# Optimization experiments

Measured on AMD Instinct MI355X. Metric: run time of the kernel, lower is better.

## Reference

```python
import jax, jax.numpy as jnp
import numpy as np
import math

NEG = -1e9
NUM_SQUEEZE = 2


def seq_mask(lengths, max_len, dtype):
    return (jnp.arange(max_len)[None, :] < lengths[:, None]).astype(dtype)


def maximum_path(logp, attn_mask, x_lengths, y_lengths):
    """Monotonic alignment search (Viterbi DP). logp, attn_mask: [B, Tx, Ty]."""
    B, Tx, Ty = logp.shape
    logp = jnp.where(attn_mask > 0, logp, NEG)
    cols = jnp.moveaxis(logp, 2, 0)  # [Ty, B, Tx]

    v0 = jnp.where(jnp.arange(Tx)[None, :] == 0, 0.0, NEG).astype(logp.dtype)
    v0 = jnp.broadcast_to(v0, (B, Tx))

    def fwd(v, col):
        v_shift = jnp.concatenate([jnp.full((B, 1), NEG, logp.dtype), v[:, :-1]], axis=1)
        v_new = col + jnp.maximum(v, v_shift)
        return v_new, v_new

    _, values = jax.lax.scan(fwd, v0, cols)  # [Ty, B, Tx] DP table

    def bwd(index, j):
        active = j < y_lengths  # [B]
        row = jax.nn.one_hot(index, Tx, dtype=logp.dtype) * active[:, None].astype(logp.dtype)
        vprev = values[jnp.maximum(j - 1, 0)]  # [B, Tx]
        v_here = jnp.take_along_axis(vprev, index[:, None], axis=1)[:, 0]
        v_left = jnp.take_along_axis(vprev, jnp.maximum(index - 1, 0)[:, None], axis=1)[:, 0]
        dec = (index != 0) & ((index == j) | (v_here < v_left)) & active & (j > 0)
        return jnp.where(dec, index - 1, index), row

    js = jnp.arange(Ty - 1, -1, -1)
    _, rows = jax.lax.scan(bwd, x_lengths - 1, js)  # reversed j order
    path = jnp.moveaxis(jnp.flip(rows, 0), 0, 2)  # [B, Tx, Ty]
    return path * attn_mask


def setup_inputs() -> dict:
    key = jax.random.key(0)
    ks = jax.random.split(key, 6)
    B, C, Ten, Tde = 32, 80, 512, 2048
    return {
        "o_mean": jax.random.normal(ks[0], (B, C, Ten), jnp.float32),
        "o_log_scale": jax.random.normal(ks[1], (B, C, Ten), jnp.float32) * 0.1,
        "o_dur_log": jax.random.normal(ks[2], (B, 1, Ten), jnp.float32),
        "z": jax.random.normal(ks[3], (B, C, Tde), jnp.float32),
        "x_lengths": jax.random.randint(ks[4], (B,), Ten // 2, Ten + 1, jnp.int32),
        "y_lengths": jax.random.randint(ks[5], (B,), Tde // 2, Tde + 1, jnp.int32),
    }


def reference(o_mean, o_log_scale, o_dur_log, z, x_lengths, y_lengths):
    B, C, Ten = o_mean.shape
    Tde = z.shape[2]
    dt = o_mean.dtype

    # preprocess: floor y_lengths to multiple of num_squeeze
    y_lengths = (y_lengths // NUM_SQUEEZE) * NUM_SQUEEZE

    x_mask = seq_mask(x_lengths, Ten, dt)[:, None, :]   # [B,1,Tx]
    y_mask = seq_mask(y_lengths, Tde, dt)[:, None, :]   # [B,1,Ty]
    attn_mask = x_mask[:, 0, :, None] * y_mask[:, 0, None, :]  # [B,Tx,Ty]

    z = z * y_mask  # decoder output is masked

    # log-likelihood terms (torch.no_grad in original)
    o_scale = jnp.exp(-2.0 * o_log_scale)                       # [B,C,Tx]
    logp1 = jnp.sum(-0.5 * math.log(2 * math.pi) - o_log_scale, axis=1)[:, :, None]
    logp2 = jnp.einsum('bct,bcs->bts', o_scale, -0.5 * z * z)   # [B,Tx,Ty]
    logp3 = jnp.einsum('bct,bcs->bts', o_mean * o_scale, z)
    logp4 = jnp.sum(-0.5 * o_mean * o_mean * o_scale, axis=1)[:, :, None]
    logp = logp1 + logp2 + logp3 + logp4

    attn = maximum_path(logp, attn_mask, x_lengths, y_lengths)  # [B,Tx,Ty] hard path

    # compute_outputs
    y_mean = jnp.einsum('bts,bct->bcs', attn, o_mean)           # [B,C,Ty]
    y_log_scale = jnp.einsum('bts,bct->bcs', attn, o_log_scale)
    o_attn_dur = jnp.log1p(jnp.sum(attn, axis=-1))[:, None, :] * x_mask  # [B,1,Tx]

    return (
        jnp.transpose(z, (0, 2, 1)),            # z: [B,Ty,C]
        jnp.transpose(y_mean, (0, 2, 1)),       # y_mean: [B,Ty,C]
        jnp.transpose(y_log_scale, (0, 2, 1)),  # y_log_scale: [B,Ty,C]
        jnp.transpose(attn, (0, 2, 1)),         # alignments: [B,Ty,Tx]
        jnp.transpose(o_dur_log, (0, 2, 1)),    # durations_log: [B,Tx,1]
        jnp.transpose(o_attn_dur, (0, 2, 1)),   # total_durations_log: [B,Tx,1]
    )
```

## Files before the change

kernel.cpp:

```cpp
#include <hip/hip_runtime.h>
#include <math.h>

#define BB  32
#define CC  80
#define TXX 512
#define TYY 2048
#define NEGV -1e9f

typedef float v2f __attribute__((ext_vector_type(2)));

__global__ __launch_bounds__(256) void k_prep(
    const float* __restrict__ om, const float* __restrict__ ols,
    float* __restrict__ SA, float* __restrict__ SB,
    float* __restrict__ L1, float* __restrict__ L4,
    float* __restrict__ OMTf, float* __restrict__ OLSTf)
{
    int b = blockIdx.y;
    int t0 = blockIdx.x * 64;
    int tid = threadIdx.x;
    int cl = tid >> 6;
    int tl = tid & 63;
    __shared__ float sm[64][81], sl[64][81], ssa[64][81];
    #pragma unroll
    for (int cp = 0; cp < 20; ++cp) {
        int c = cp * 4 + cl;
        size_t gidx = ((size_t)b * CC + c) * TXX + t0 + tl;
        float m = om[gidx], ls = ols[gidx];
        float sa = expf(-2.0f * ls);
        SA[gidx] = sa;
        SB[gidx] = m * sa;
        sm[tl][c] = m; sl[tl][c] = ls; ssa[tl][c] = sa;
    }
    __syncthreads();
    if (tid < 64) {
        float l1 = 0.f, l4 = 0.f;
        #pragma unroll 4
        for (int c = 0; c < CC; ++c) {
            float m = sm[tid][c], ls = sl[tid][c], sa = ssa[tid][c];
            l1 += (-0.9189385332046727f - ls);
            l4 += ((-0.5f * m) * m) * sa;
        }
        int g = b * TXX + t0 + tid;
        L1[g] = l1; L4[g] = l4;
    }
    size_t obase = (size_t)b * TXX * CC + (size_t)t0 * CC;
    for (int e = tid; e < 64 * CC; e += 256) {
        int t = e / CC, c = e - t * CC;
        OMTf[obase + e]  = sm[t][c];
        OLSTf[obase + e] = sl[t][c];
    }
}

__global__ __launch_bounds__(256) void k_logp(
    const float* __restrict__ SA, const float* __restrict__ SB,
    const float* __restrict__ L1, const float* __restrict__ L4,
    const float* __restrict__ z,
    const int* __restrict__ xlp, const int* __restrict__ ylp,
    float* __restrict__ logp)
{
    int b = blockIdx.z;
    int ylen = (ylp[b] >> 1) << 1;
    int s0 = blockIdx.y * 128;
    if (s0 >= ylen) return;
    int t0 = blockIdx.x * 64;
    int xlen = xlp[b];
    int tid = threadIdx.x;

    __shared__ float sA[16][64], sB[16][64], sZ[16][128], sW[16][128];

    v2f acc2[4][4], acc3[4][4];
    #pragma unroll
    for (int i = 0; i < 4; ++i)
        #pragma unroll
        for (int p = 0; p < 4; ++p) { acc2[i][p] = (v2f){0.f, 0.f}; acc3[i][p] = (v2f){0.f, 0.f}; }

    int tt = (tid & 15) << 2;
    int ss = (tid >> 4) << 3;
    int r  = tid >> 4;
    int c4 = (tid & 15) << 2;
    int s8 = (tid & 15) << 3;

    for (int c0 = 0; c0 < CC; c0 += 16) {
        const float* pa = SA + ((size_t)b * CC + (c0 + r)) * TXX + t0 + c4;
        const float* pb = SB + ((size_t)b * CC + (c0 + r)) * TXX + t0 + c4;
        float4 va = *(const float4*)pa;
        float4 vb = *(const float4*)pb;
        *(float4*)&sA[r][c4] = va;
        *(float4*)&sB[r][c4] = vb;

        const float* pz = z + ((size_t)b * CC + (c0 + r)) * TYY + s0 + s8;
        float4 q0 = *(const float4*)pz;
        float4 q1 = *(const float4*)(pz + 4);
        float zf[8] = {q0.x, q0.y, q0.z, q0.w, q1.x, q1.y, q1.z, q1.w};
        #pragma unroll
        for (int i = 0; i < 8; ++i) {
            sZ[r][s8 + i] = zf[i];
            sW[r][s8 + i] = (-0.5f * zf[i]) * zf[i];
        }
        __syncthreads();
        #pragma unroll
        for (int kc = 0; kc < 16; ++kc) {
            float4 a2 = *(const float4*)&sA[kc][tt];
            float4 a3 = *(const float4*)&sB[kc][tt];
            const v2f* zp = (const v2f*)&sZ[kc][ss];
            const v2f* wp = (const v2f*)&sW[kc][ss];
            v2f bz[4] = {zp[0], zp[1], zp[2], zp[3]};
            v2f bw[4] = {wp[0], wp[1], wp[2], wp[3]};
            float av2[4] = {a2.x, a2.y, a2.z, a2.w};
            float av3[4] = {a3.x, a3.y, a3.z, a3.w};
            #pragma unroll
            for (int i = 0; i < 4; ++i) {
                v2f d2 = {av2[i], av2[i]};
                v2f d3 = {av3[i], av3[i]};
                #pragma unroll
                for (int p = 0; p < 4; ++p) {
                    acc2[i][p] = __builtin_elementwise_fma(d2, bw[p], acc2[i][p]);
                    acc3[i][p] = __builtin_elementwise_fma(d3, bz[p], acc3[i][p]);
                }
            }
        }
        __syncthreads();
    }

    float l1a[4], l4a[4]; int bad[4];
    #pragma unroll
    for (int i = 0; i < 4; ++i) {
        int t = t0 + tt + i;
        l1a[i] = L1[b * TXX + t];
        l4a[i] = L4[b * TXX + t];
        bad[i] = (t >= xlen);
    }
    #pragma unroll
    for (int p = 0; p < 4; ++p) {
        #pragma unroll
        for (int h = 0; h < 2; ++h) {
            int s = s0 + ss + 2 * p + h;
            float vals[4];
            #pragma unroll
            for (int i = 0; i < 4; ++i) {
                float a2v = h ? acc2[i][p].y : acc2[i][p].x;
                float a3v = h ? acc3[i][p].y : acc3[i][p].x;
                float v = ((l1a[i] + a2v) + a3v) + l4a[i];
                vals[i] = bad[i] ? NEGV : v;
            }
            float4 o; o.x = vals[0]; o.y = vals[1]; o.z = vals[2]; o.w = vals[3];
            *(float4*)&logp[((size_t)b * TYY + s) * TXX + t0 + tt] = o;
        }
    }
}

__global__ __launch_bounds__(512) void k_fwd(
    const float* __restrict__ logp, const int* __restrict__ ylp,
    unsigned long long* __restrict__ BITS64)
{
    int b = blockIdx.x;
    int tid = threadIdx.x;
    int w = tid >> 6, lane = tid & 63;
    int n = (ylp[b] >> 1) << 1;
    int nm1 = n - 1;
    int nb = (n + 63) >> 6;
    const float* lpt = logp + (size_t)b * TYY * TXX + tid;
    unsigned long long* bout = BITS64 + ((size_t)b * 8 + w) * TYY;

    __shared__ float bnd[8][4][64];

    float v = (tid == 0) ? 0.0f : NEGV;
    float c[16];
    unsigned blo = 0u, bhi = 0u;
    int rounds = nb + 7;
    for (int r = 0; r < rounds; ++r) {
        int blk = r - w;
        if (blk >= 0 && blk < nb) {
            int S0 = blk << 6;
            if (blk == 0) {
                #pragma unroll
                for (int i = 0; i < 16; ++i) c[i] = lpt[(size_t)i * TXX];
            }
            float BL;
            if (w == 0) {
                BL = NEGV;
            } else {
                const float* srcp = (lane == 0) ? &bnd[w - 1][(blk + 3) & 3][63]
                                                : &bnd[w - 1][blk & 3][lane - 1];
                BL = *srcp;
                if (blk == 0 && lane == 0) BL = NEGV;
            }
            float BLout = 0.0f;
            #pragma unroll
            for (int j = 0; j < 64; ++j) {
                float cc = c[j & 15];
                int ps = S0 + j + 16; ps = (ps > nm1) ? nm1 : ps;
                c[j & 15] = lpt[(size_t)ps * TXX];
                int blj = (int)__builtin_amdgcn_readlane(__float_as_uint(BL), j);
                float left = __uint_as_float((unsigned)__builtin_amdgcn_update_dpp(
                    blj, (int)__float_as_uint(v), 0x138 , 0xf, 0xf, false));
                unsigned long long m = __ballot(v < left);
                bool me = (lane == j);
                blo = me ? (unsigned)m : blo;
                bhi = me ? (unsigned)(m >> 32) : bhi;
                v = cc + fmaxf(v, left);
                float v63 = __uint_as_float(
                    __builtin_amdgcn_readlane(__float_as_uint(v), 63));
                BLout = me ? v63 : BLout;
            }
            bnd[w][blk & 3][lane] = BLout;
            int row = S0 - 1 + lane;
            if (row >= 0 && S0 + lane < n)
                bout[row] = (((unsigned long long)bhi) << 32) | blo;
        }
        __syncthreads();
    }
}

__global__ __launch_bounds__(64) void k_bwd(
    const unsigned long long* __restrict__ BITS64, const int* __restrict__ xlp,
    const int* __restrict__ ylp, int* __restrict__ TSTAR)
{
    int b = blockIdx.x, lane = threadIdx.x;
    int ylen = (ylp[b] >> 1) << 1;
    int xlen = xlp[b];
    const unsigned long long* bb = BITS64 + (size_t)b * 8 * TYY;
    int* tst = TSTAR + b * TYY;

    int idx = xlen - 1;
    int j_hi = ylen - 1;

    while (j_hi >= 63) {
        int e = idx >> 6;
        int base_w = (e > 0) ? (e - 1) : 0;
        int base_bit = base_w << 6;
        int row = j_hi - 1 - lane;
        unsigned long long wl = 0ull, wh = 0ull;
        if (row >= 0) {
            wl = bb[(size_t)base_w * TYY + row];
            wh = bb[(size_t)(base_w + 1) * TYY + row];
        }
        unsigned wl0 = (unsigned)wl, wl1 = (unsigned)(wl >> 32);
        unsigned wh0 = (unsigned)wh, wh1 = (unsigned)(wh >> 32);
        int acc = 0;
        int pos = idx - base_bit;
        #pragma unroll
        for (int k = 0; k < 64; ++k) {
            int j = j_hi - k;
            unsigned a0 = __builtin_amdgcn_readlane(wl0, k);
            unsigned a1 = __builtin_amdgcn_readlane(wl1, k);
            unsigned c0 = __builtin_amdgcn_readlane(wh0, k);
            unsigned c1 = __builtin_amdgcn_readlane(wh1, k);
            unsigned long long wkl = ((unsigned long long)a1 << 32) | a0;
            unsigned long long wkh = ((unsigned long long)c1 << 32) | c0;
            unsigned long long sel = (pos & 64) ? wkh : wkl;
            unsigned bit = (unsigned)(sel >> (pos & 63)) & 1u;
            int idxv = pos + base_bit;
            acc = (lane == k) ? idxv : acc;
            int dec = (idxv != 0 && j > 0 && (idxv == j || bit)) ? 1 : 0;
            pos -= dec;
        }
        idx = pos + base_bit;
        tst[j_hi - lane] = acc;
        j_hi -= 64;
    }
    if (j_hi >= 0) {
        int steps = j_hi + 1;
        int e = idx >> 6;
        int base_w = (e > 0) ? (e - 1) : 0;
        int base_bit = base_w << 6;
        int row = j_hi - 1 - lane;
        unsigned long long wl = 0ull, wh = 0ull;
        if (row >= 0) {
            wl = bb[(size_t)base_w * TYY + row];
            wh = bb[(size_t)(base_w + 1) * TYY + row];
        }
        unsigned wl0 = (unsigned)wl, wl1 = (unsigned)(wl >> 32);
        unsigned wh0 = (unsigned)wh, wh1 = (unsigned)(wh >> 32);
        int acc = 0;
        int pos = idx - base_bit;
        for (int k = 0; k < steps; ++k) {
            int j = j_hi - k;
            unsigned a0 = __builtin_amdgcn_readlane(wl0, k);
            unsigned a1 = __builtin_amdgcn_readlane(wl1, k);
            unsigned c0 = __builtin_amdgcn_readlane(wh0, k);
            unsigned c1 = __builtin_amdgcn_readlane(wh1, k);
            unsigned long long wkl = ((unsigned long long)a1 << 32) | a0;
            unsigned long long wkh = ((unsigned long long)c1 << 32) | c0;
            unsigned long long sel = (pos & 64) ? wkh : wkl;
            unsigned bit = (unsigned)(sel >> (pos & 63)) & 1u;
            int idxv = pos + base_bit;
            acc = (lane == k) ? idxv : acc;
            int dec = (idxv != 0 && j > 0 && (idxv == j || bit)) ? 1 : 0;
            pos -= dec;
        }
        if (lane < steps) tst[j_hi - lane] = acc;
    }
}

__device__ __forceinline__ int lbound2048(const int* __restrict__ ts, int n, int x)
{
    int pos = 0;
    #pragma unroll
    for (int step = 2048; step >= 1; step >>= 1) {
        int np = pos + step;
        if (np <= n && ts[np - 1] < x) pos = np;
    }
    return pos;
}

__global__ __launch_bounds__(256) void k_small(
    const float* __restrict__ odur, const int* __restrict__ xlp,
    const int* __restrict__ ylp, const int* __restrict__ TSTAR,
    float* __restrict__ out4, float* __restrict__ out5)
{
    int gid = blockIdx.x * 256 + threadIdx.x;
    int b = gid >> 9, t = gid & 511;
    out4[gid] = odur[gid];
    int xlen = xlp[b];
    int ylen = (ylp[b] >> 1) << 1;
    const int* ts = TSTAR + b * TYY;
    float r = 0.0f;
    if (t < xlen) {
        int lo = lbound2048(ts, ylen, t);
        int hi = lbound2048(ts, ylen, t + 1);
        r = log1pf((float)(hi - lo));
    }
    out5[gid] = r;
}

__global__ __launch_bounds__(256) void k_out_sc(
    const float* __restrict__ z, const float* __restrict__ OMTf,
    const float* __restrict__ OLSTf, const int* __restrict__ TSTAR,
    const int* __restrict__ ylp,
    float* __restrict__ out0, float* __restrict__ out1,
    float* __restrict__ out2)
{
    int b = blockIdx.y;
    int s0 = blockIdx.x * 32;
    int tid = threadIdx.x;
    int ylen = (ylp[b] >> 1) << 1;
    __shared__ int sT[32];
    __shared__ float zt[32][81];
    if (tid < 32) {
        int s = s0 + tid;
        sT[tid] = (s < ylen) ? TSTAR[b * TYY + s] : 0;
    }
    int c_l = tid >> 5, s_l = tid & 31;
    #pragma unroll
    for (int cp = 0; cp < 10; ++cp) {
        int c = cp * 8 + c_l;
        zt[s_l][c] = z[((size_t)b * CC + c) * TYY + s0 + s_l];
    }
    __syncthreads();
    for (int e = tid; e < 32 * 80; e += 256) {
        int sl = e / 80;
        int cc = e - sl * 80;
        int s = s0 + sl;
        bool valid = s < ylen;
        int t = sT[sl];
        size_t o = ((size_t)b * TYY + s) * 80 + cc;
        size_t g = ((size_t)b * TXX + t) * 80 + cc;
        out0[o] = valid ? zt[sl][cc] : 0.0f;
        out1[o] = valid ? OMTf[g]    : 0.0f;
        out2[o] = valid ? OLSTf[g]   : 0.0f;
    }
}

__global__ __launch_bounds__(256) void k_attn(
    const int* __restrict__ TSTAR, const int* __restrict__ ylp,
    float* __restrict__ out3)
{
    int b = blockIdx.y;
    int s0 = blockIdx.x * 16;
    int tid = threadIdx.x;
    int ylen = (ylp[b] >> 1) << 1;
    #pragma unroll
    for (int r = 0; r < 16; ++r) {
        int s = s0 + r;
        int tr = (s < ylen) ? TSTAR[b * TYY + s] : -1;
        int t = tid << 1;
        float2 val;
        val.x = (t == tr) ? 1.0f : 0.0f;
        val.y = (t + 1 == tr) ? 1.0f : 0.0f;
        ((float2*)(out3 + ((size_t)b * TYY + s) * TXX))[tid] = val;
    }
}

extern "C" void kernel_launch(void* const* d_in, const int* in_sizes, int n_in,
                              void* d_out, int out_size, void* d_ws, size_t ws_size,
                              hipStream_t stream)
{
    const float* om   = (const float*)d_in[0];
    const float* ols  = (const float*)d_in[1];
    const float* odur = (const float*)d_in[2];
    const float* z    = (const float*)d_in[3];
    const int* xl = (const int*)d_in[4];
    const int* yl = (const int*)d_in[5];

    float* out0 = (float*)d_out;
    float* out1 = out0 + 5242880;
    float* out2 = out0 + 10485760;
    float* out3 = out0 + 15728640;
    float* out4 = out0 + 49283072;
    float* out5 = out0 + 49299456;

    float* SA   = out0;
    float* SB   = out0 + 1310720;
    float* logp = out3;

    char* ws = (char*)d_ws;
    float* L1 = (float*)ws;
    float* L4 = (float*)(ws + 65536);
    float* OMTf  = (float*)(ws + 131072);
    float* OLSTf = (float*)(ws + 5373952);
    unsigned long long* BITS64 = (unsigned long long*)(ws + 10616832);
    int* TSTAR = (int*)(ws + 14811136);

    hipLaunchKernelGGL(k_prep, dim3(8, 32), dim3(256), 0, stream,
                       om, ols, SA, SB, L1, L4, OMTf, OLSTf);
    hipLaunchKernelGGL(k_logp, dim3(8, 16, 32), dim3(256), 0, stream,
                       SA, SB, L1, L4, z, xl, yl, logp);
    hipLaunchKernelGGL(k_fwd, dim3(32), dim3(512), 0, stream, logp, yl, BITS64);
    hipLaunchKernelGGL(k_bwd, dim3(32), dim3(64), 0, stream, BITS64, xl, yl, TSTAR);
    hipLaunchKernelGGL(k_small, dim3(64), dim3(256), 0, stream, odur, xl, yl, TSTAR, out4, out5);
    hipLaunchKernelGGL(k_out_sc, dim3(64, 32), dim3(256), 0, stream,
                       z, OMTf, OLSTf, TSTAR, yl, out0, out1, out2);
    hipLaunchKernelGGL(k_attn, dim3(128, 32), dim3(256), 0, stream, TSTAR, yl, out3);
}
```

Measured before the change: 646.7 us.

## Process two Tx positions per lane in Viterbi forward, repack decision bits separately

Measured after the change: 883.8 us. 1.37x slower.

```diff
diff --git a/kernel.cpp b/kernel.cpp
--- a/kernel.cpp
+++ b/kernel.cpp
@@ -6,6 +6,7 @@
 #define TXX 512
 #define TYY 2048
 #define NEGV -1e9f
+#define PF  32
 
 typedef float v2f __attribute__((ext_vector_type(2)));
 
@@ -149,9 +150,9 @@
     }
 }
 
-__global__ __launch_bounds__(512) void k_fwd(
+__global__ __launch_bounds__(256) void k_fwd(
     const float* __restrict__ logp, const int* __restrict__ ylp,
-    unsigned long long* __restrict__ BITS64)
+    unsigned long long* __restrict__ BITSP)
 {
     int b = blockIdx.x;
     int tid = threadIdx.x;
@@ -159,22 +160,26 @@
     int n = (ylp[b] >> 1) << 1;
     int nm1 = n - 1;
     int nb = (n + 63) >> 6;
-    const float* lpt = logp + (size_t)b * TYY * TXX + tid;
-    unsigned long long* bout = BITS64 + ((size_t)b * 8 + w) * TYY;
-
-    __shared__ float bnd[8][4][64];
-
-    float v = (tid == 0) ? 0.0f : NEGV;
-    float c[16];
-    unsigned blo = 0u, bhi = 0u;
-    int rounds = nb + 7;
+    const float* lpb = logp + (size_t)b * TYY * TXX;
+    int coff = (w << 7) + (lane << 1);
+    unsigned long long* boutE = BITSP + ((size_t)b * 8 + 2 * w) * TYY;
+    unsigned long long* boutO = boutE + TYY;
+
+    __shared__ float bnd[4][4][64];
+
+    float vlo = (tid == 0) ? 0.0f : NEGV;
+    float vhi = NEGV;
+    float2 c[PF];
+    unsigned eLo = 0u, eHi = 0u, oLo = 0u, oHi = 0u;
+    int rounds = nb + 3;
     for (int r = 0; r < rounds; ++r) {
         int blk = r - w;
         if (blk >= 0 && blk < nb) {
             int S0 = blk << 6;
             if (blk == 0) {
                 #pragma unroll
-                for (int i = 0; i < 16; ++i) c[i] = lpt[(size_t)i * TXX];
+                for (int i = 0; i < PF; ++i)
+                    c[i] = *(const float2*)(lpb + (size_t)i * TXX + coff);
             }
             float BL;
             if (w == 0) {
@@ -188,28 +193,67 @@
             float BLout = 0.0f;
             #pragma unroll
             for (int j = 0; j < 64; ++j) {
-                float cc = c[j & 15];
-                int ps = S0 + j + 16; ps = (ps > nm1) ? nm1 : ps;
-                c[j & 15] = lpt[(size_t)ps * TXX];
+                float2 cc = c[j & (PF - 1)];
+                int ps = S0 + j + PF; ps = (ps > nm1) ? nm1 : ps;
+                c[j & (PF - 1)] = *(const float2*)(lpb + (size_t)ps * TXX + coff);
                 int blj = (int)__builtin_amdgcn_readlane(__float_as_uint(BL), j);
                 float left = __uint_as_float((unsigned)__builtin_amdgcn_update_dpp(
-                    blj, (int)__float_as_uint(v), 0x138 , 0xf, 0xf, false));
-                unsigned long long m = __ballot(v < left);
+                    blj, (int)__float_as_uint(vhi), 0x138 , 0xf, 0xf, false));
+                unsigned long long mE = __ballot(vlo < left);
+                unsigned long long mO = __ballot(vhi < vlo);
                 bool me = (lane == j);
-                blo = me ? (unsigned)m : blo;
-                bhi = me ? (unsigned)(m >> 32) : bhi;
-                v = cc + fmaxf(v, left);
+                eLo = me ? (unsigned)mE : eLo;
+                eHi = me ? (unsigned)(mE >> 32) : eHi;
+                oLo = me ? (unsigned)mO : oLo;
+                oHi = me ? (unsigned)(mO >> 32) : oHi;
+                float nlo = cc.x + fmaxf(vlo, left);
+                float nhi = cc.y + fmaxf(vhi, vlo);
+                vlo = nlo; vhi = nhi;
                 float v63 = __uint_as_float(
-                    __builtin_amdgcn_readlane(__float_as_uint(v), 63));
+                    __builtin_amdgcn_readlane(__float_as_uint(vhi), 63));
                 BLout = me ? v63 : BLout;
             }
             bnd[w][blk & 3][lane] = BLout;
             int row = S0 - 1 + lane;
-            if (row >= 0 && S0 + lane < n)
-                bout[row] = (((unsigned long long)bhi) << 32) | blo;
-        }
-        __syncthreads();
-    }
+            if (row >= 0 && S0 + lane < n) {
+                boutE[row] = (((unsigned long long)eHi) << 32) | eLo;
+                boutO[row] = (((unsigned long long)oHi) << 32) | oLo;
+            }
+        }
+        asm volatile("s_waitcnt lgkmcnt(0)" ::: "memory");
+        __builtin_amdgcn_s_barrier();
+        asm volatile("" ::: "memory");
+    }
+}
+
+__device__ __forceinline__ unsigned long long spread32(unsigned x)
+{
+    unsigned long long v = x;
+    v = (v | (v << 16)) & 0x0000FFFF0000FFFFull;
+    v = (v | (v << 8))  & 0x00FF00FF00FF00FFull;
+    v = (v | (v << 4))  & 0x0F0F0F0F0F0F0F0Full;
+    v = (v | (v << 2))  & 0x3333333333333333ull;
+    v = (v | (v << 1))  & 0x5555555555555555ull;
+    return v;
+}
+
+__global__ __launch_bounds__(256) void k_rp(
+    const unsigned long long* __restrict__ BITSP,
+    unsigned long long* __restrict__ BITS64)
+{
+    int gid = blockIdx.x * 256 + threadIdx.x;
+    int b = gid >> 13;
+    int rem = gid & 8191;
+    int wp = rem >> 11;
+    int row = rem & 2047;
+    const unsigned long long* src = BITSP + ((size_t)b * 8 + 2 * wp) * TYY + row;
+    unsigned long long e = src[0];
+    unsigned long long o = src[TYY];
+    unsigned long long w0 = spread32((unsigned)e) | (spread32((unsigned)o) << 1);
+    unsigned long long w1 = spread32((unsigned)(e >> 32)) | (spread32((unsigned)(o >> 32)) << 1);
+    unsigned long long* dst = BITS64 + ((size_t)b * 8 + 2 * wp) * TYY + row;
+    dst[0] = w0;
+    dst[TYY] = w1;
 }
 
 __global__ __launch_bounds__(64) void k_bwd(
@@ -403,6 +447,7 @@
     float* SA   = out0;
     float* SB   = out0 + 1310720;
     float* logp = out3;
+    unsigned long long* BITSP = (unsigned long long*)out1;
 
     char* ws = (char*)d_ws;
     float* L1 = (float*)ws;
@@ -416,7 +461,8 @@
                        om, ols, SA, SB, L1, L4, OMTf, OLSTf);
     hipLaunchKernelGGL(k_logp, dim3(8, 16, 32), dim3(256), 0, stream,
                        SA, SB, L1, L4, z, xl, yl, logp);
-    hipLaunchKernelGGL(k_fwd, dim3(32), dim3(512), 0, stream, logp, yl, BITS64);
+    hipLaunchKernelGGL(k_fwd, dim3(32), dim3(256), 0, stream, logp, yl, BITSP);
+    hipLaunchKernelGGL(k_rp, dim3(1024), dim3(256), 0, stream, BITSP, BITS64);
     hipLaunchKernelGGL(k_bwd, dim3(32), dim3(64), 0, stream, BITS64, xl, yl, TSTAR);
     hipLaunchKernelGGL(k_small, dim3(64), dim3(256), 0, stream, odur, xl, yl, TSTAR, out4, out5);
     hipLaunchKernelGGL(k_out_sc, dim3(64, 32), dim3(256), 0, stream,
```

## Restructure Viterbi forward as single-wave with 8 columns per lane

Applied to the files above, without the earlier changes.

Measured after the change: 793.3 us. 1.23x slower.

```diff
diff --git a/kernel.cpp b/kernel.cpp
--- a/kernel.cpp
+++ b/kernel.cpp
@@ -64,6 +64,7 @@
     if (s0 >= ylen) return;
     int t0 = blockIdx.x * 64;
     int xlen = xlp[b];
+    if (t0 >= xlen) return;
     int tid = threadIdx.x;
 
     __shared__ float sA[16][64], sB[16][64], sZ[16][128], sW[16][128];
@@ -149,77 +150,106 @@
     }
 }
 
-__global__ __launch_bounds__(512) void k_fwd(
+#define KF_ROW(JJ, S) { \
+    float4 ca = ra[S], cb = rb[S]; \
+    int pf = (JJ) + 16; pf = (pf > nm1) ? nm1 : pf; \
+    ra[S] = *(const float4*)(lp + (size_t)pf * TXX); \
+    rb[S] = *(const float4*)(lp + (size_t)pf * TXX + 4); \
+    float l0 = __uint_as_float((unsigned)__builtin_amdgcn_update_dpp( \
+        (int)__float_as_uint(NEGR), (int)__float_as_uint(v7), 0x138, 0xf, 0xf, false)); \
+    unsigned by_ = (v0 < l0) ? 1u : 0u; \
+    by_ |= (v1 < v0) ? 2u : 0u; \
+    by_ |= (v2 < v1) ? 4u : 0u; \
+    by_ |= (v3 < v2) ? 8u : 0u; \
+    by_ |= (v4 < v3) ? 16u : 0u; \
+    by_ |= (v5 < v4) ? 32u : 0u; \
+    by_ |= (v6 < v5) ? 64u : 0u; \
+    by_ |= (v7 < v6) ? 128u : 0u; \
+    byp[(size_t)((JJ) - 1) * 64] = (unsigned char)by_; \
+    float nv0 = ca.x + fmaxf(v0, l0); \
+    float nv1 = ca.y + fmaxf(v1, v0); \
+    float nv2 = ca.z + fmaxf(v2, v1); \
+    float nv3 = ca.w + fmaxf(v3, v2); \
+    float nv4 = cb.x + fmaxf(v4, v3); \
+    float nv5 = cb.y + fmaxf(v5, v4); \
+    float nv6 = cb.z + fmaxf(v6, v5); \
+    float nv7 = cb.w + fmaxf(v7, v6); \
+    v0 = nv0; v1 = nv1; v2 = nv2; v3 = nv3; \
+    v4 = nv4; v5 = nv5; v6 = nv6; v7 = nv7; \
+}
+
+__global__ __launch_bounds__(64) void k_fwd(
     const float* __restrict__ logp, const int* __restrict__ ylp,
-    unsigned long long* __restrict__ BITS64)
+    unsigned char* __restrict__ BYTES)
 {
     int b = blockIdx.x;
-    int tid = threadIdx.x;
-    int w = tid >> 6, lane = tid & 63;
+    int lane = threadIdx.x;
     int n = (ylp[b] >> 1) << 1;
     int nm1 = n - 1;
-    int nb = (n + 63) >> 6;
-    const float* lpt = logp + (size_t)b * TYY * TXX + tid;
-    unsigned long long* bout = BITS64 + ((size_t)b * 8 + w) * TYY;
-
-    __shared__ float bnd[8][4][64];
-
-    float v = (tid == 0) ? 0.0f : NEGV;
-    float c[16];
-    unsigned blo = 0u, bhi = 0u;
-    int rounds = nb + 7;
-    for (int r = 0; r < rounds; ++r) {
-        int blk = r - w;
-        if (blk >= 0 && blk < nb) {
-            int S0 = blk << 6;
-            if (blk == 0) {
-                #pragma unroll
-                for (int i = 0; i < 16; ++i) c[i] = lpt[(size_t)i * TXX];
-            }
-            float BL;
-            if (w == 0) {
-                BL = NEGV;
-            } else {
-                const float* srcp = (lane == 0) ? &bnd[w - 1][(blk + 3) & 3][63]
-                                                : &bnd[w - 1][blk & 3][lane - 1];
-                BL = *srcp;
-                if (blk == 0 && lane == 0) BL = NEGV;
-            }
-            float BLout = 0.0f;
-            #pragma unroll
-            for (int j = 0; j < 64; ++j) {
-                float cc = c[j & 15];
-                int ps = S0 + j + 16; ps = (ps > nm1) ? nm1 : ps;
-                c[j & 15] = lpt[(size_t)ps * TXX];
-                int blj = (int)__builtin_amdgcn_readlane(__float_as_uint(BL), j);
-                float left = __uint_as_float((unsigned)__builtin_amdgcn_update_dpp(
-                    blj, (int)__float_as_uint(v), 0x138 , 0xf, 0xf, false));
-                unsigned long long m = __ballot(v < left);
-                bool me = (lane == j);
-                blo = me ? (unsigned)m : blo;
-                bhi = me ? (unsigned)(m >> 32) : bhi;
-                v = cc + fmaxf(v, left);
-                float v63 = __uint_as_float(
-                    __builtin_amdgcn_readlane(__float_as_uint(v), 63));
-                BLout = me ? v63 : BLout;
-            }
-            bnd[w][blk & 3][lane] = BLout;
-            int row = S0 - 1 + lane;
-            if (row >= 0 && S0 + lane < n)
-                bout[row] = (((unsigned long long)bhi) << 32) | blo;
-        }
-        __syncthreads();
-    }
+    const float* lp = logp + (size_t)b * TYY * TXX + lane * 8;
+    unsigned char* byp = BYTES + (size_t)b * TYY * 64 + lane;
+    float NEGR = NEGV;
+
+    float4 ra[16], rb[16];
+    #pragma unroll
+    for (int i = 0; i < 16; ++i) {
+        ra[i] = *(const float4*)(lp + (size_t)i * TXX);
+        rb[i] = *(const float4*)(lp + (size_t)i * TXX + 4);
+    }
+
+    float v0 = (lane == 0) ? 0.0f : NEGV;
+    float v1 = NEGV, v2 = NEGV, v3 = NEGV, v4 = NEGV, v5 = NEGV, v6 = NEGV, v7 = NEGV;
+
+    {
+        float4 ca = ra[0], cb = rb[0];
+        ra[0] = *(const float4*)(lp + (size_t)16 * TXX);
+        rb[0] = *(const float4*)(lp + (size_t)16 * TXX + 4);
+        float l0 = __uint_as_float((unsigned)__builtin_amdgcn_update_dpp(
+            (int)__float_as_uint(NEGR), (int)__float_as_uint(v7), 0x138, 0xf, 0xf, false));
+        float nv0 = ca.x + fmaxf(v0, l0);
+        float nv1 = ca.y + fmaxf(v1, v0);
+        float nv2 = ca.z + fmaxf(v2, v1);
+        float nv3 = ca.w + fmaxf(v3, v2);
+        float nv4 = cb.x + fmaxf(v4, v3);
+        float nv5 = cb.y + fmaxf(v5, v4);
+        float nv6 = cb.z + fmaxf(v6, v5);
+        float nv7 = cb.w + fmaxf(v7, v6);
+        v0 = nv0; v1 = nv1; v2 = nv2; v3 = nv3;
+        v4 = nv4; v5 = nv5; v6 = nv6; v7 = nv7;
+    }
+
+    int j = 1;
+    for (; j + 16 <= n; j += 16) {
+        KF_ROW(j + 0, 1)  KF_ROW(j + 1, 2)  KF_ROW(j + 2, 3)  KF_ROW(j + 3, 4)
+        KF_ROW(j + 4, 5)  KF_ROW(j + 5, 6)  KF_ROW(j + 6, 7)  KF_ROW(j + 7, 8)
+        KF_ROW(j + 8, 9)  KF_ROW(j + 9, 10) KF_ROW(j + 10, 11) KF_ROW(j + 11, 12)
+        KF_ROW(j + 12, 13) KF_ROW(j + 13, 14) KF_ROW(j + 14, 15) KF_ROW(j + 15, 0)
+    }
+    if (j + 0  < n) KF_ROW(j + 0, 1)
+    if (j + 1  < n) KF_ROW(j + 1, 2)
+    if (j + 2  < n) KF_ROW(j + 2, 3)
+    if (j + 3  < n) KF_ROW(j + 3, 4)
+    if (j + 4  < n) KF_ROW(j + 4, 5)
+    if (j + 5  < n) KF_ROW(j + 5, 6)
+    if (j + 6  < n) KF_ROW(j + 6, 7)
+    if (j + 7  < n) KF_ROW(j + 7, 8)
+    if (j + 8  < n) KF_ROW(j + 8, 9)
+    if (j + 9  < n) KF_ROW(j + 9, 10)
+    if (j + 10 < n) KF_ROW(j + 10, 11)
+    if (j + 11 < n) KF_ROW(j + 11, 12)
+    if (j + 12 < n) KF_ROW(j + 12, 13)
+    if (j + 13 < n) KF_ROW(j + 13, 14)
+    if (j + 14 < n) KF_ROW(j + 14, 15)
 }
 
 __global__ __launch_bounds__(64) void k_bwd(
-    const unsigned long long* __restrict__ BITS64, const int* __restrict__ xlp,
+    const unsigned char* __restrict__ BYTES, const int* __restrict__ xlp,
     const int* __restrict__ ylp, int* __restrict__ TSTAR)
 {
     int b = blockIdx.x, lane = threadIdx.x;
     int ylen = (ylp[b] >> 1) << 1;
     int xlen = xlp[b];
-    const unsigned long long* bb = BITS64 + (size_t)b * 8 * TYY;
+    const unsigned char* bybase = BYTES + (size_t)b * TYY * 64;
     int* tst = TSTAR + b * TYY;
 
     int idx = xlen - 1;
@@ -227,13 +257,15 @@
 
     while (j_hi >= 63) {
         int e = idx >> 6;
-        int base_w = (e > 0) ? (e - 1) : 0;
-        int base_bit = base_w << 6;
+        int q0 = (e > 0) ? (e - 1) : 0;
+        int base_bit = q0 << 6;
         int row = j_hi - 1 - lane;
         unsigned long long wl = 0ull, wh = 0ull;
         if (row >= 0) {
-            wl = bb[(size_t)base_w * TYY + row];
-            wh = bb[(size_t)(base_w + 1) * TYY + row];
+            const unsigned long long* rp =
+                (const unsigned long long*)(bybase + (size_t)row * 64);
+            wl = rp[q0];
+            wh = rp[q0 + 1];
         }
         unsigned wl0 = (unsigned)wl, wl1 = (unsigned)(wl >> 32);
         unsigned wh0 = (unsigned)wh, wh1 = (unsigned)(wh >> 32);
@@ -262,13 +294,15 @@
     if (j_hi >= 0) {
         int steps = j_hi + 1;
         int e = idx >> 6;
-        int base_w = (e > 0) ? (e - 1) : 0;
-        int base_bit = base_w << 6;
+        int q0 = (e > 0) ? (e - 1) : 0;
+        int base_bit = q0 << 6;
         int row = j_hi - 1 - lane;
         unsigned long long wl = 0ull, wh = 0ull;
         if (row >= 0) {
-            wl = bb[(size_t)base_w * TYY + row];
-            wh = bb[(size_t)(base_w + 1) * TYY + row];
+            const unsigned long long* rp =
+                (const unsigned long long*)(bybase + (size_t)row * 64);
+            wl = rp[q0];
+            wh = rp[q0 + 1];
         }
         unsigned wl0 = (unsigned)wl, wl1 = (unsigned)(wl >> 32);
         unsigned wh0 = (unsigned)wh, wh1 = (unsigned)(wh >> 32);
@@ -409,15 +443,15 @@
     float* L4 = (float*)(ws + 65536);
     float* OMTf  = (float*)(ws + 131072);
     float* OLSTf = (float*)(ws + 5373952);
-    unsigned long long* BITS64 = (unsigned long long*)(ws + 10616832);
+    unsigned char* BYTES = (unsigned char*)(ws + 10616832);
     int* TSTAR = (int*)(ws + 14811136);
 
     hipLaunchKernelGGL(k_prep, dim3(8, 32), dim3(256), 0, stream,
                        om, ols, SA, SB, L1, L4, OMTf, OLSTf);
     hipLaunchKernelGGL(k_logp, dim3(8, 16, 32), dim3(256), 0, stream,
                        SA, SB, L1, L4, z, xl, yl, logp);
-    hipLaunchKernelGGL(k_fwd, dim3(32), dim3(512), 0, stream, logp, yl, BITS64);
-    hipLaunchKernelGGL(k_bwd, dim3(32), dim3(64), 0, stream, BITS64, xl, yl, TSTAR);
+    hipLaunchKernelGGL(k_fwd, dim3(32), dim3(64), 0, stream, logp, yl, BYTES);
+    hipLaunchKernelGGL(k_bwd, dim3(32), dim3(64), 0, stream, BYTES, xl, yl, TSTAR);
     hipLaunchKernelGGL(k_small, dim3(64), dim3(256), 0, stream, odur, xl, yl, TSTAR, out4, out5);
     hipLaunchKernelGGL(k_out_sc, dim3(64, 32), dim3(256), 0, stream,
                        z, OMTf, OLSTf, TSTAR, yl, out0, out1, out2);
```
